# Kernel tuning notes

Measured on AMD Instinct MI355X. Metric: run time of the kernel, lower is better.

Reference implementation:

```python
import jax, jax.numpy as jnp
import numpy as np

CONSTRAINT_WEIGHT = 0.5
FOCAL_GAMMA = 2.0
EPS = 1e-8

B, G, C = 65536, 9, 9
BLK = 3  # int(sqrt(G))


def setup_inputs() -> dict:
    key = jax.random.key(0)
    k1, k2, k3 = jax.random.split(key, 3)
    logits = jax.random.normal(k1, (B, G, G, C), dtype=jnp.float32)
    targets = jax.random.randint(k2, (B, G, G), 0, 10, dtype=jnp.int64)
    puzzles = jax.random.randint(k3, (B, G, G), 0, 10, dtype=jnp.int64)
    return {"logits": logits, "targets": targets, "puzzles": puzzles}


def _sudoku_loss(logits, targets, puzzles):
    b, g, _, c = logits.shape
    mask = (puzzles == 0).astype(logits.dtype)            # [B,G,G]
    tgt = jnp.clip(targets - 1, 0, c - 1)                 # [B,G,G]

    log_probs = jax.nn.log_softmax(logits, axis=-1)       # [B,G,G,C]
    probs = jnp.exp(log_probs)

    # --- focal CE over masked (empty) cells ---
    lp_t = jnp.take_along_axis(log_probs, tgt[..., None], axis=-1)[..., 0]  # [B,G,G]
    pt = jnp.exp(lp_t)
    ce = -lp_t
    focal = (1.0 - pt) ** FOCAL_GAMMA * ce
    msum = mask.sum()
    ce_loss = (focal * mask).sum() / (msum + EPS)

    # --- constraint loss ---
    masked_probs = probs * mask[..., None]                # [B,G,G,C]
    row_sums = masked_probs.sum(axis=2)                   # [B,G,C]
    row_loss = jnp.mean((row_sums - 1.0) ** 2)
    col_sums = masked_probs.sum(axis=1)                   # [B,G,C]
    col_loss = jnp.mean((col_sums - 1.0) ** 2)
    # boxes: [B, br, r, bc, c_in, C] -> sum over the 3x3 cells of each box
    box = masked_probs.reshape(b, BLK, BLK, BLK, BLK, c)
    box_sums = box.transpose(0, 1, 3, 2, 4, 5).reshape(b, BLK * BLK, BLK * BLK, c).sum(axis=2)
    box_loss = jnp.mean((box_sums - 1.0) ** 2)

    entropy = -(probs * log_probs).sum(axis=-1)           # [B,G,G]
    entropy_loss = 0.1 * ((entropy * mask).sum() / (msum + EPS))

    top2, _ = jax.lax.top_k(probs, 2)                     # [B,G,G,2]
    gap = top2[..., 0] - top2[..., 1]
    uniqueness_loss = 0.1 * jnp.mean(jax.nn.relu(1.0 - gap))

    constraint_loss = (row_loss + col_loss + box_loss + entropy_loss + uniqueness_loss) * 0.2
    return ce_loss + CONSTRAINT_WEIGHT * constraint_loss


def reference(logits, targets, puzzles):
    return _sudoku_loss(logits, targets, puzzles)
```

## Files before the change

kernel.cpp:

```cpp
#include <hip/hip_runtime.h>

#define THREADS 256
#define PB 12
#define CELLS_PB (PB * 81)
#define WORKERS 243
#define TOTW (CELLS_PB * 9)

typedef float f4 __attribute__((ext_vector_type(4)));
typedef __fp16 h2 __attribute__((ext_vector_type(2)));
typedef unsigned int u32;
typedef int i4 __attribute__((ext_vector_type(4)));

static __device__ __forceinline__ u32 pkrtz(float a, float b) {
  h2 v = __builtin_amdgcn_cvt_pkrtz(a, b);
  return __builtin_bit_cast(u32, v);
}

__global__ __launch_bounds__(THREADS) void sudoku_main(
    const float* __restrict__ logits,
    const int*   __restrict__ targets,
    const int*   __restrict__ puzzles,
    float* __restrict__ partial,
    int B, int ngrid)
{
  __shared__ float buf[TOTW];
  __shared__ float sred[4][5];

  const int tid = threadIdx.x;
  const int g   = blockIdx.x;
  const long totalCells = (long)B * 81;

  float a_focal=0.f, a_ent=0.f, a_msk=0.f, a_uniq=0.f, a_sq=0.f;

  if (tid < WORKERS) {
    const size_t gbase4 = (size_t)g * (TOTW / 4);
    const size_t lim4   = (size_t)(totalCells * 9 / 4);
    const f4* src = (const f4*)logits;
#pragma unroll
    for (int r = 0; r < 9; ++r) {
      size_t idx = gbase4 + r * WORKERS + tid;
      if (idx < lim4) ((f4*)buf)[r * WORKERS + tid] = src[idx];
    }
  }

  const long cell0 = (long)g * CELLS_PB + 4 * tid;
  const bool vA = (tid < WORKERS) && (cell0 < totalCells);
  i4 tg4{}, pz4{};
  if (vA) {
    tg4 = *(const i4*)(targets + cell0);
    pz4 = *(const i4*)(puzzles + cell0);
  }
  __syncthreads();

  if (vA) {
    f4 s[9];
#pragma unroll
    for (int q = 0; q < 9; ++q) s[q] = ((const f4*)buf)[tid * 9 + q];

#pragma unroll
    for (int k = 0; k < 4; ++k) {
      float l[9];
#pragma unroll
      for (int i = 0; i < 9; ++i) { const int w = 9 * k + i; l[i] = s[w >> 2][w & 3]; }
      int tg = tg4[k] - 1; tg = tg < 0 ? 0 : (tg > 8 ? 8 : tg);

      float t1 = l[0], t2 = -3.0e38f;
#pragma unroll
      for (int i = 1; i < 9; ++i) {
        float hi = fmaxf(t1, l[i]);
        float lo = fminf(t1, l[i]);
        t1 = hi; t2 = fmaxf(t2, lo);
      }
      float e[9], ssum = 0.f, lsum = 0.f, ltg = l[0];
#pragma unroll
      for (int i = 0; i < 9; ++i) {
        float x  = l[i] - t1;
        float ei = __expf(x);
        e[i] = ei; ssum += ei;
        lsum = fmaf(ei, x, lsum);
        if (i > 0) ltg = (tg == i) ? l[i] : ltg;
      }
      float inv_s = __builtin_amdgcn_rcpf(ssum);
      float logs  = __logf(ssum);
      float lpt   = (ltg - t1) - logs;
      float pt    = __expf(lpt);
      float om    = 1.f - pt;
      float focal = om * om * (-lpt);
      float ent   = logs - lsum * inv_s;
      float gap   = (1.f - __expf(t2 - t1)) * inv_s;
      float uq    = fmaxf(0.f, 1.f - gap);
      float mk    = (pz4[k] == 0) ? 1.f : 0.f;
      a_focal += focal * mk;
      a_ent   += ent * mk;
      a_msk   += mk;
      a_uniq  += uq;
      float pm = inv_s * mk;

      u32* pw = (u32*)buf + (size_t)(4 * tid + k) * 9;
      pw[0] = pkrtz(e[0] * pm, e[1] * pm);
      pw[1] = pkrtz(e[2] * pm, e[3] * pm);
      pw[2] = pkrtz(e[4] * pm, e[5] * pm);
      pw[3] = pkrtz(e[6] * pm, e[7] * pm);
      pw[4] = pkrtz(e[8] * pm, 0.f);
    }
  }
  __syncthreads();

  if (tid < PB * 5) {
    const int pz = tid / 5, pr = tid - 5 * pz;
    if ((long)g * PB + pz < B) {
      const u32* cb = (const u32*)buf;
      h2 hz; hz[0] = (__fp16)0.f; hz[1] = (__fp16)0.f;
      h2 rs[9], cs[9], bs[9];
#pragma unroll
      for (int u = 0; u < 9; ++u) { rs[u] = hz; cs[u] = hz; bs[u] = hz; }
      const int base = pz * 729 + pr;
#pragma unroll
      for (int j = 0; j < 81; ++j) {
        h2 v = __builtin_bit_cast(h2, cb[base + 9 * j]);
        rs[j / 9]                    += v;
        cs[j % 9]                    += v;
        bs[(j / 27) * 3 + (j % 9) / 3] += v;
      }
      const float hiw = (pr == 4) ? 0.f : 1.f;
      float sq = 0.f;
#pragma unroll
      for (int u = 0; u < 9; ++u) {
        float x;
        x = (float)rs[u][0] - 1.f; sq = fmaf(x, x, sq);
        x = (float)cs[u][0] - 1.f; sq = fmaf(x, x, sq);
        x = (float)bs[u][0] - 1.f; sq = fmaf(x, x, sq);
        x = (float)rs[u][1] - 1.f; sq = fmaf(hiw * x, x, sq);
        x = (float)cs[u][1] - 1.f; sq = fmaf(hiw * x, x, sq);
        x = (float)bs[u][1] - 1.f; sq = fmaf(hiw * x, x, sq);
      }
      a_sq += sq;
    }
  }

#pragma unroll
  for (int off = 32; off > 0; off >>= 1) {
    a_focal += __shfl_down(a_focal, off);
    a_ent   += __shfl_down(a_ent,   off);
    a_msk   += __shfl_down(a_msk,   off);
    a_uniq  += __shfl_down(a_uniq,  off);
    a_sq    += __shfl_down(a_sq,    off);
  }
  const int wv = tid >> 6, lane = tid & 63;
  if (lane == 0) {
    sred[wv][0] = a_focal; sred[wv][1] = a_ent; sred[wv][2] = a_msk;
    sred[wv][3] = a_uniq;  sred[wv][4] = a_sq;
  }
  __syncthreads();
  if (tid < 5) {
    float v = sred[0][tid] + sred[1][tid] + sred[2][tid] + sred[3][tid];
    partial[(size_t)tid * ngrid + g] = v;
  }
}

__global__ __launch_bounds__(1024) void sudoku_finalize(
    const float* __restrict__ partial, float* __restrict__ out,
    int ngrid, float invBG)
{
  __shared__ float sb[16][5];
  const int tid = threadIdx.x;
  float s[5] = {0.f, 0.f, 0.f, 0.f, 0.f};
  for (int b = tid; b < ngrid; b += 1024) {
#pragma unroll
    for (int u = 0; u < 5; ++u) s[u] += partial[(size_t)u * ngrid + b];
  }
#pragma unroll
  for (int off = 32; off > 0; off >>= 1)
#pragma unroll
    for (int u = 0; u < 5; ++u) s[u] += __shfl_down(s[u], off);
  const int wv = tid >> 6, lane = tid & 63;
  if (lane == 0) {
#pragma unroll
    for (int u = 0; u < 5; ++u) sb[wv][u] = s[u];
  }
  __syncthreads();
  if (tid == 0) {
    float focal = 0.f, ent = 0.f, msum = 0.f, uniq = 0.f, sq = 0.f;
#pragma unroll
    for (int w = 0; w < 16; ++w) {
      focal += sb[w][0]; ent += sb[w][1]; msum += sb[w][2];
      uniq  += sb[w][3]; sq  += sb[w][4];
    }
    float inv_m = 1.f / (msum + 1e-8f);
    float ce    = focal * inv_m;
    float entl  = 0.1f * ent * inv_m;
    float uql   = 0.1f * uniq * invBG;
    float rcb   = sq * invBG;
    float constraint = (rcb + entl + uql) * 0.2f;
    out[0] = ce + 0.5f * constraint;
  }
}

extern "C" void kernel_launch(void* const* d_in, const int* in_sizes, int n_in,
                              void* d_out, int out_size, void* d_ws, size_t ws_size,
                              hipStream_t stream)
{
  (void)n_in; (void)out_size; (void)ws_size;
  const float* logits  = (const float*)d_in[0];
  const int*   targets = (const int*)d_in[1];
  const int*   puzzles = (const int*)d_in[2];
  float* out = (float*)d_out;
  float* partial = (float*)d_ws;

  const int B = in_sizes[0] / 729;
  const long totalCells = (long)B * 81;
  const int ngrid = (int)((totalCells + CELLS_PB - 1) / CELLS_PB);

  sudoku_main<<<ngrid, THREADS, 0, stream>>>(logits, targets, puzzles, partial, B, ngrid);

  const float invBG = 1.f / ((float)B * 81.f);
  sudoku_finalize<<<1, 1024, 0, stream>>>(partial, out, ngrid, invBG);
}
```

Baseline: 57.20 us.

## Replace LDS staging with per-row lane mapping and wavefront shuffle reductions

Each wavefront lane now owns one puzzle row (9 cells) and loads its logits straight from global memory, dropping the shared-memory staging buffer and both block barriers. Row sums are done in registers. Column and box sums use packed-fp16 shuffle-down reductions across lanes. The trade-off is unaligned, strided per-lane loads (each lane reads a 324-byte row segment), which coalesce less well than the old linear f4 copy. It also adds high register pressure (45 packed halves per lane), one idle lane per wave, and many cross-lane shuffles.

```diff
diff --git a/kernel.cpp b/kernel.cpp
--- a/kernel.cpp
+++ b/kernel.cpp
@@ -1,19 +1,28 @@
 #include <hip/hip_runtime.h>
 
 #define THREADS 256
-#define PB 12
-#define CELLS_PB (PB * 81)
-#define WORKERS 243
-#define TOTW (CELLS_PB * 9)
+#define WPP 7
 
 typedef float f4 __attribute__((ext_vector_type(4)));
+typedef f4 f4a4 __attribute__((aligned(4)));
+typedef int i4 __attribute__((ext_vector_type(4)));
+typedef i4 i4a4 __attribute__((aligned(4)));
 typedef __fp16 h2 __attribute__((ext_vector_type(2)));
 typedef unsigned int u32;
-typedef int i4 __attribute__((ext_vector_type(4)));
-
-static __device__ __forceinline__ u32 pkrtz(float a, float b) {
-  h2 v = __builtin_amdgcn_cvt_pkrtz(a, b);
-  return __builtin_bit_cast(u32, v);
+
+static __device__ __forceinline__ h2 shd_h2(h2 v, int d) {
+  u32 x = __builtin_bit_cast(u32, v);
+  x = __shfl_down(x, d);
+  return __builtin_bit_cast(h2, x);
+}
+static __device__ __forceinline__ h2 red9(h2 v) {
+  h2 t = v + shd_h2(v, 1);
+  t = t + shd_h2(t, 2);
+  t = t + shd_h2(t, 4);
+  return t + shd_h2(v, 8);
+}
+static __device__ __forceinline__ h2 red3(h2 v) {
+  return v + shd_h2(v, 1) + shd_h2(v, 2);
 }
 
 __global__ __launch_bounds__(THREADS) void sudoku_main(
@@ -21,48 +30,43 @@
     const int*   __restrict__ targets,
     const int*   __restrict__ puzzles,
     float* __restrict__ partial,
-    int B, int ngrid)
+    int B, int nblk)
 {
-  __shared__ float buf[TOTW];
   __shared__ float sred[4][5];
 
-  const int tid = threadIdx.x;
-  const int g   = blockIdx.x;
-  const long totalCells = (long)B * 81;
+  const int tid  = threadIdx.x;
+  const int wv   = tid >> 6, lane = tid & 63;
+  const long wpass = (long)blockIdx.x * 4 + wv;
+  const int o    = lane % 9;
+  const int pzl  = lane / 9;
+  const long pzG = wpass * WPP + pzl;
+  const bool valid = (lane < 63) && (pzG < (long)B);
 
   float a_focal=0.f, a_ent=0.f, a_msk=0.f, a_uniq=0.f, a_sq=0.f;
 
-  if (tid < WORKERS) {
-    const size_t gbase4 = (size_t)g * (TOTW / 4);
-    const size_t lim4   = (size_t)(totalCells * 9 / 4);
-    const f4* src = (const f4*)logits;
-#pragma unroll
-    for (int r = 0; r < 9; ++r) {
-      size_t idx = gbase4 + r * WORKERS + tid;
-      if (idx < lim4) ((f4*)buf)[r * WORKERS + tid] = src[idx];
-    }
-  }
-
-  const long cell0 = (long)g * CELLS_PB + 4 * tid;
-  const bool vA = (tid < WORKERS) && (cell0 < totalCells);
-  i4 tg4{}, pz4{};
-  if (vA) {
-    tg4 = *(const i4*)(targets + cell0);
-    pz4 = *(const i4*)(puzzles + cell0);
-  }
-  __syncthreads();
-
-  if (vA) {
-    f4 s[9];
-#pragma unroll
-    for (int q = 0; q < 9; ++q) s[q] = ((const f4*)buf)[tid * 9 + q];
-
-#pragma unroll
-    for (int k = 0; k < 4; ++k) {
-      float l[9];
-#pragma unroll
-      for (int i = 0; i < 9; ++i) { const int w = 9 * k + i; l[i] = s[w >> 2][w & 3]; }
-      int tg = tg4[k] - 1; tg = tg < 0 ? 0 : (tg > 8 ? 8 : tg);
+  h2 p45[45];
+  {
+    h2 hz; hz[0] = (__fp16)0.f; hz[1] = (__fp16)0.f;
+#pragma unroll
+    for (int i = 0; i < 45; ++i) p45[i] = hz;
+  }
+
+  if (valid) {
+    const long cellBase = pzG * 81 + (long)o * 9;
+    const float* fb = logits + cellBase * 9;
+    const int*  tb  = targets + cellBase;
+    const int*  pb  = puzzles + cellBase;
+    i4 tg0 = *(const i4a4*)tb, tg1 = *(const i4a4*)(tb + 4);
+    i4 pz0 = *(const i4a4*)pb, pz1 = *(const i4a4*)(pb + 4);
+    const int tgs[9] = {tg0[0],tg0[1],tg0[2],tg0[3],tg1[0],tg1[1],tg1[2],tg1[3],tb[8]};
+    const int pzs[9] = {pz0[0],pz0[1],pz0[2],pz0[3],pz1[0],pz1[1],pz1[2],pz1[3],pb[8]};
+
+#pragma unroll
+    for (int k = 0; k < 9; ++k) {
+      f4 va = *(const f4a4*)(fb + 9 * k);
+      f4 vb = *(const f4a4*)(fb + 9 * k + 4);
+      float l[9] = {va[0],va[1],va[2],va[3],vb[0],vb[1],vb[2],vb[3], fb[9*k+8]};
+      int tg = tgs[k] - 1; tg = tg < 0 ? 0 : (tg > 8 ? 8 : tg);
 
       float t1 = l[0], t2 = -3.0e38f;
 #pragma unroll
@@ -89,52 +93,53 @@
       float ent   = logs - lsum * inv_s;
       float gap   = (1.f - __expf(t2 - t1)) * inv_s;
       float uq    = fmaxf(0.f, 1.f - gap);
-      float mk    = (pz4[k] == 0) ? 1.f : 0.f;
+      float mk    = (pzs[k] == 0) ? 1.f : 0.f;
       a_focal += focal * mk;
       a_ent   += ent * mk;
       a_msk   += mk;
       a_uniq  += uq;
       float pm = inv_s * mk;
-
-      u32* pw = (u32*)buf + (size_t)(4 * tid + k) * 9;
-      pw[0] = pkrtz(e[0] * pm, e[1] * pm);
-      pw[1] = pkrtz(e[2] * pm, e[3] * pm);
-      pw[2] = pkrtz(e[4] * pm, e[5] * pm);
-      pw[3] = pkrtz(e[6] * pm, e[7] * pm);
-      pw[4] = pkrtz(e[8] * pm, 0.f);
-    }
-  }
-  __syncthreads();
-
-  if (tid < PB * 5) {
-    const int pz = tid / 5, pr = tid - 5 * pz;
-    if ((long)g * PB + pz < B) {
-      const u32* cb = (const u32*)buf;
-      h2 hz; hz[0] = (__fp16)0.f; hz[1] = (__fp16)0.f;
-      h2 rs[9], cs[9], bs[9];
-#pragma unroll
-      for (int u = 0; u < 9; ++u) { rs[u] = hz; cs[u] = hz; bs[u] = hz; }
-      const int base = pz * 729 + pr;
-#pragma unroll
-      for (int j = 0; j < 81; ++j) {
-        h2 v = __builtin_bit_cast(h2, cb[base + 9 * j]);
-        rs[j / 9]                    += v;
-        cs[j % 9]                    += v;
-        bs[(j / 27) * 3 + (j % 9) / 3] += v;
-      }
-      const float hiw = (pr == 4) ? 0.f : 1.f;
-      float sq = 0.f;
-#pragma unroll
-      for (int u = 0; u < 9; ++u) {
-        float x;
-        x = (float)rs[u][0] - 1.f; sq = fmaf(x, x, sq);
-        x = (float)cs[u][0] - 1.f; sq = fmaf(x, x, sq);
-        x = (float)bs[u][0] - 1.f; sq = fmaf(x, x, sq);
-        x = (float)rs[u][1] - 1.f; sq = fmaf(hiw * x, x, sq);
-        x = (float)cs[u][1] - 1.f; sq = fmaf(hiw * x, x, sq);
-        x = (float)bs[u][1] - 1.f; sq = fmaf(hiw * x, x, sq);
-      }
-      a_sq += sq;
+      h2 hpm = __builtin_amdgcn_cvt_pkrtz(pm, pm);
+      p45[5*k+0] = __builtin_amdgcn_cvt_pkrtz(e[0], e[1]) * hpm;
+      p45[5*k+1] = __builtin_amdgcn_cvt_pkrtz(e[2], e[3]) * hpm;
+      p45[5*k+2] = __builtin_amdgcn_cvt_pkrtz(e[4], e[5]) * hpm;
+      p45[5*k+3] = __builtin_amdgcn_cvt_pkrtz(e[6], e[7]) * hpm;
+      p45[5*k+4] = __builtin_amdgcn_cvt_pkrtz(e[8], 0.f)  * hpm;
+    }
+
+#pragma unroll
+    for (int j = 0; j < 5; ++j) {
+      h2 s = p45[j];
+#pragma unroll
+      for (int c = 1; c < 9; ++c) s = s + p45[5*c+j];
+      float x = (float)s[0] - 1.f; a_sq = fmaf(x, x, a_sq);
+      if (j < 4) { float y = (float)s[1] - 1.f; a_sq = fmaf(y, y, a_sq); }
+    }
+  }
+
+  h2 bx[15];
+#pragma unroll
+  for (int b = 0; b < 3; ++b)
+#pragma unroll
+    for (int j = 0; j < 5; ++j)
+      bx[b*5+j] = p45[(3*b)*5+j] + p45[(3*b+1)*5+j] + p45[(3*b+2)*5+j];
+#pragma unroll
+  for (int i = 0; i < 15; ++i) bx[i] = red3(bx[i]);
+  if (valid && (o == 0 || o == 3 || o == 6)) {
+#pragma unroll
+    for (int i = 0; i < 15; ++i) {
+      float x = (float)bx[i][0] - 1.f; a_sq = fmaf(x, x, a_sq);
+      if ((i % 5) < 4) { float y = (float)bx[i][1] - 1.f; a_sq = fmaf(y, y, a_sq); }
+    }
+  }
+
+#pragma unroll
+  for (int i = 0; i < 45; ++i) p45[i] = red9(p45[i]);
+  if (valid && o == 0) {
+#pragma unroll
+    for (int i = 0; i < 45; ++i) {
+      float x = (float)p45[i][0] - 1.f; a_sq = fmaf(x, x, a_sq);
+      if ((i % 5) < 4) { float y = (float)p45[i][1] - 1.f; a_sq = fmaf(y, y, a_sq); }
     }
   }
 
@@ -146,7 +151,6 @@
     a_uniq  += __shfl_down(a_uniq,  off);
     a_sq    += __shfl_down(a_sq,    off);
   }
-  const int wv = tid >> 6, lane = tid & 63;
   if (lane == 0) {
     sred[wv][0] = a_focal; sred[wv][1] = a_ent; sred[wv][2] = a_msk;
     sred[wv][3] = a_uniq;  sred[wv][4] = a_sq;
@@ -154,20 +158,20 @@
   __syncthreads();
   if (tid < 5) {
     float v = sred[0][tid] + sred[1][tid] + sred[2][tid] + sred[3][tid];
-    partial[(size_t)tid * ngrid + g] = v;
+    partial[(size_t)tid * nblk + blockIdx.x] = v;
   }
 }
 
 __global__ __launch_bounds__(1024) void sudoku_finalize(
     const float* __restrict__ partial, float* __restrict__ out,
-    int ngrid, float invBG)
+    int nblk, float invBG)
 {
   __shared__ float sb[16][5];
   const int tid = threadIdx.x;
   float s[5] = {0.f, 0.f, 0.f, 0.f, 0.f};
-  for (int b = tid; b < ngrid; b += 1024) {
-#pragma unroll
-    for (int u = 0; u < 5; ++u) s[u] += partial[(size_t)u * ngrid + b];
+  for (int b = tid; b < nblk; b += 1024) {
+#pragma unroll
+    for (int u = 0; u < 5; ++u) s[u] += partial[(size_t)u * nblk + b];
   }
 #pragma unroll
   for (int off = 32; off > 0; off >>= 1)
@@ -208,11 +212,11 @@
   float* partial = (float*)d_ws;
 
   const int B = in_sizes[0] / 729;
-  const long totalCells = (long)B * 81;
-  const int ngrid = (int)((totalCells + CELLS_PB - 1) / CELLS_PB);
-
-  sudoku_main<<<ngrid, THREADS, 0, stream>>>(logits, targets, puzzles, partial, B, ngrid);
+  const long npass = ((long)B + WPP - 1) / WPP;
+  const int  nblk  = (int)((npass + 3) / 4);
+
+  sudoku_main<<<nblk, THREADS, 0, stream>>>(logits, targets, puzzles, partial, B, nblk);
 
   const float invBG = 1.f / ((float)B * 81.f);
-  sudoku_finalize<<<1, 1024, 0, stream>>>(partial, out, ngrid, invBG);
-}
+  sudoku_finalize<<<1, 1024, 0, stream>>>(partial, out, nblk, invBG);
+}
```

After: 69.86 us. +22.1%, slower.

## Convert to persistent grid-stride kernel with double-buffered register-prefetched logits

Applied to the files above, without the earlier changes.

Replaces one-block-per-12-puzzles launch with a persistent grid (capped at 1536 blocks) that loops over 4-puzzle chunks. Logits, targets and puzzles for the next chunk are loaded into registers while the current chunk is computed, then written to the alternate shared buffer. The constraint reduction rotates across waves per iteration. This aims to overlap global memory latency with compute and shrink the shared footprint for higher occupancy, but adds more barriers per unit of work and smaller per-iteration parallelism.

```diff
diff --git a/kernel.cpp b/kernel.cpp
--- a/kernel.cpp
+++ b/kernel.cpp
@@ -1,15 +1,18 @@
 #include <hip/hip_runtime.h>
 
 #define THREADS 256
-#define PB 12
-#define CELLS_PB (PB * 81)
-#define WORKERS 243
-#define TOTW (CELLS_PB * 9)
+#define CPZ 4
+#define CC (CPZ * 81)
+#define CW (CC * 9)
+#define CF4 (CW / 4)
+#define MAXG 1536
 
 typedef float f4 __attribute__((ext_vector_type(4)));
+typedef float f2 __attribute__((ext_vector_type(2)));
+typedef int   i2 __attribute__((ext_vector_type(2)));
 typedef __fp16 h2 __attribute__((ext_vector_type(2)));
 typedef unsigned int u32;
-typedef int i4 __attribute__((ext_vector_type(4)));
+typedef u32 u2 __attribute__((ext_vector_type(2)));
 
 static __device__ __forceinline__ u32 pkrtz(float a, float b) {
   h2 v = __builtin_amdgcn_cvt_pkrtz(a, b);
@@ -21,121 +24,160 @@
     const int*   __restrict__ targets,
     const int*   __restrict__ puzzles,
     float* __restrict__ partial,
-    int B, int ngrid)
+    int B, long nchunk, int grid)
 {
-  __shared__ float buf[TOTW];
+  __shared__ float buf[2][CW];
   __shared__ float sred[4][5];
 
-  const int tid = threadIdx.x;
-  const int g   = blockIdx.x;
+  const int tid  = threadIdx.x;
+  const int wv   = tid >> 6, lane = tid & 63;
   const long totalCells = (long)B * 81;
+  const long totF4      = totalCells * 9 / 4;
+  const bool stager  = tid < 243;
 
   float a_focal=0.f, a_ent=0.f, a_msk=0.f, a_uniq=0.f, a_sq=0.f;
 
-  if (tid < WORKERS) {
-    const size_t gbase4 = (size_t)g * (TOTW / 4);
-    const size_t lim4   = (size_t)(totalCells * 9 / 4);
+  const long c0 = blockIdx.x;
+  if (stager) {
     const f4* src = (const f4*)logits;
-#pragma unroll
-    for (int r = 0; r < 9; ++r) {
-      size_t idx = gbase4 + r * WORKERS + tid;
-      if (idx < lim4) ((f4*)buf)[r * WORKERS + tid] = src[idx];
-    }
-  }
-
-  const long cell0 = (long)g * CELLS_PB + 4 * tid;
-  const bool vA = (tid < WORKERS) && (cell0 < totalCells);
-  i4 tg4{}, pz4{};
-  if (vA) {
-    tg4 = *(const i4*)(targets + cell0);
-    pz4 = *(const i4*)(puzzles + cell0);
-  }
-  __syncthreads();
-
-  if (vA) {
-    f4 s[9];
-#pragma unroll
-    for (int q = 0; q < 9; ++q) s[q] = ((const f4*)buf)[tid * 9 + q];
-
-#pragma unroll
-    for (int k = 0; k < 4; ++k) {
-      float l[9];
-#pragma unroll
-      for (int i = 0; i < 9; ++i) { const int w = 9 * k + i; l[i] = s[w >> 2][w & 3]; }
-      int tg = tg4[k] - 1; tg = tg < 0 ? 0 : (tg > 8 ? 8 : tg);
-
-      float t1 = l[0], t2 = -3.0e38f;
-#pragma unroll
-      for (int i = 1; i < 9; ++i) {
-        float hi = fmaxf(t1, l[i]);
-        float lo = fminf(t1, l[i]);
-        t1 = hi; t2 = fmaxf(t2, lo);
+    const long b4 = c0 * CF4;
+#pragma unroll
+    for (int r = 0; r < 3; ++r) {
+      long idx = b4 + r * 243 + tid;
+      if (idx < totF4) ((f4*)buf[0])[r * 243 + tid] = src[idx];
+    }
+  }
+  bool vA = false; i2 tgc{}, pzc{};
+  {
+    const long cell0 = c0 * CC + 2 * tid;
+    vA = (tid < 162) && (cell0 + 1 < totalCells);
+    if (vA) { tgc = *(const i2*)(targets + cell0); pzc = *(const i2*)(puzzles + cell0); }
+  }
+
+  int it = 0;
+  for (long c = c0; c < nchunk; c += grid, ++it) {
+    float* X = buf[it & 1];
+    float* Y = buf[(it & 1) ^ 1];
+    __syncthreads();
+
+    const long cn = c + grid;
+    f4 r0{}, r1{}, r2{};
+    const bool vS = stager && (cn < nchunk);
+    if (vS) {
+      const f4* src = (const f4*)logits;
+      const long b4 = cn * CF4;
+      long i0 = b4 + tid, i1 = b4 + 243 + tid, ii2 = b4 + 486 + tid;
+      if (i0  < totF4) r0 = src[i0];
+      if (i1  < totF4) r1 = src[i1];
+      if (ii2 < totF4) r2 = src[ii2];
+    }
+    bool vAn = false; i2 tgn{}, pzn{};
+    if (cn < nchunk) {
+      const long cell0n = cn * CC + 2 * tid;
+      vAn = (tid < 162) && (cell0n + 1 < totalCells);
+      if (vAn) { tgn = *(const i2*)(targets + cell0n); pzn = *(const i2*)(puzzles + cell0n); }
+    }
+
+    if (vA) {
+      f2 v[9];
+      const f2* xp = (const f2*)(X + 18 * tid);
+#pragma unroll
+      for (int q = 0; q < 9; ++q) v[q] = xp[q];
+
+      u32 q5[2][5];
+#pragma unroll
+      for (int k = 0; k < 2; ++k) {
+        float l[9];
+#pragma unroll
+        for (int i = 0; i < 9; ++i) { const int w = 9 * k + i; l[i] = v[w >> 1][w & 1]; }
+        int tg = ((k == 0) ? tgc[0] : tgc[1]) - 1; tg = tg < 0 ? 0 : (tg > 8 ? 8 : tg);
+        const int pz = (k == 0) ? pzc[0] : pzc[1];
+
+        float t1 = l[0], t2 = -3.0e38f;
+#pragma unroll
+        for (int i = 1; i < 9; ++i) {
+          float hi = fmaxf(t1, l[i]);
+          float lo = fminf(t1, l[i]);
+          t1 = hi; t2 = fmaxf(t2, lo);
+        }
+        float e[9], ssum = 0.f, lsum = 0.f, ltg = l[0];
+#pragma unroll
+        for (int i = 0; i < 9; ++i) {
+          float x  = l[i] - t1;
+          float ei = __expf(x);
+          e[i] = ei; ssum += ei;
+          lsum = fmaf(ei, x, lsum);
+          if (i > 0) ltg = (tg == i) ? l[i] : ltg;
+        }
+        float inv_s = __builtin_amdgcn_rcpf(ssum);
+        float logs  = __logf(ssum);
+        float lpt   = (ltg - t1) - logs;
+        float pt    = __expf(lpt);
+        float om    = 1.f - pt;
+        float focal = om * om * (-lpt);
+        float ent   = logs - lsum * inv_s;
+        float gap   = (1.f - __expf(t2 - t1)) * inv_s;
+        float uq    = fmaxf(0.f, 1.f - gap);
+        float mk    = (pz == 0) ? 1.f : 0.f;
+        a_focal += focal * mk;
+        a_ent   += ent * mk;
+        a_msk   += mk;
+        a_uniq  += uq;
+        float pm = inv_s * mk;
+        q5[k][0] = pkrtz(e[0]*pm, e[1]*pm);
+        q5[k][1] = pkrtz(e[2]*pm, e[3]*pm);
+        q5[k][2] = pkrtz(e[4]*pm, e[5]*pm);
+        q5[k][3] = pkrtz(e[6]*pm, e[7]*pm);
+        q5[k][4] = pkrtz(e[8]*pm, 0.f);
       }
-      float e[9], ssum = 0.f, lsum = 0.f, ltg = l[0];
-#pragma unroll
-      for (int i = 0; i < 9; ++i) {
-        float x  = l[i] - t1;
-        float ei = __expf(x);
-        e[i] = ei; ssum += ei;
-        lsum = fmaf(ei, x, lsum);
-        if (i > 0) ltg = (tg == i) ? l[i] : ltg;
+      u32* wp = (u32*)(X + 18 * tid);
+      { u2 a; a[0]=q5[0][0]; a[1]=q5[0][1]; *(u2*)(wp + 0) = a; }
+      { u2 a; a[0]=q5[0][2]; a[1]=q5[0][3]; *(u2*)(wp + 2) = a; }
+      wp[4] = q5[0][4];
+      wp[9] = q5[1][0];
+      { u2 a; a[0]=q5[1][1]; a[1]=q5[1][2]; *(u2*)(wp + 10) = a; }
+      { u2 a; a[0]=q5[1][3]; a[1]=q5[1][4]; *(u2*)(wp + 12) = a; }
+    }
+
+    if (vS) {
+      f4* yp = (f4*)Y;
+      yp[tid] = r0; yp[243 + tid] = r1; yp[486 + tid] = r2;
+    }
+    __syncthreads();
+
+    if (wv == (it & 3) && lane < CPZ * 5) {
+      const int pzl = lane / 5, pr = lane % 5;
+      if (c * CPZ + pzl < (long)B) {
+        const u32* cb = (const u32*)X;
+        h2 hz; hz[0] = (__fp16)0.f; hz[1] = (__fp16)0.f;
+        h2 rs[9], cs[9], bs[9];
+#pragma unroll
+        for (int u = 0; u < 9; ++u) { rs[u] = hz; cs[u] = hz; bs[u] = hz; }
+        const int base = pzl * 729 + pr;
+#pragma unroll
+        for (int j = 0; j < 81; ++j) {
+          h2 pv = __builtin_bit_cast(h2, cb[base + 9 * j]);
+          rs[j / 9]                      += pv;
+          cs[j % 9]                      += pv;
+          bs[(j / 27) * 3 + (j % 9) / 3] += pv;
+        }
+        const float hiw = (pr == 4) ? 0.f : 1.f;
+        float sq = 0.f;
+#pragma unroll
+        for (int u = 0; u < 9; ++u) {
+          float x;
+          x = (float)rs[u][0] - 1.f; sq = fmaf(x, x, sq);
+          x = (float)cs[u][0] - 1.f; sq = fmaf(x, x, sq);
+          x = (float)bs[u][0] - 1.f; sq = fmaf(x, x, sq);
+          x = (float)rs[u][1] - 1.f; sq = fmaf(hiw * x, x, sq);
+          x = (float)cs[u][1] - 1.f; sq = fmaf(hiw * x, x, sq);
+          x = (float)bs[u][1] - 1.f; sq = fmaf(hiw * x, x, sq);
+        }
+        a_sq += sq;
       }
-      float inv_s = __builtin_amdgcn_rcpf(ssum);
-      float logs  = __logf(ssum);
-      float lpt   = (ltg - t1) - logs;
-      float pt    = __expf(lpt);
-      float om    = 1.f - pt;
-      float focal = om * om * (-lpt);
-      float ent   = logs - lsum * inv_s;
-      float gap   = (1.f - __expf(t2 - t1)) * inv_s;
-      float uq    = fmaxf(0.f, 1.f - gap);
-      float mk    = (pz4[k] == 0) ? 1.f : 0.f;
-      a_focal += focal * mk;
-      a_ent   += ent * mk;
-      a_msk   += mk;
-      a_uniq  += uq;
-      float pm = inv_s * mk;
-
-      u32* pw = (u32*)buf + (size_t)(4 * tid + k) * 9;
-      pw[0] = pkrtz(e[0] * pm, e[1] * pm);
-      pw[1] = pkrtz(e[2] * pm, e[3] * pm);
-      pw[2] = pkrtz(e[4] * pm, e[5] * pm);
-      pw[3] = pkrtz(e[6] * pm, e[7] * pm);
-      pw[4] = pkrtz(e[8] * pm, 0.f);
-    }
-  }
-  __syncthreads();
-
-  if (tid < PB * 5) {
-    const int pz = tid / 5, pr = tid - 5 * pz;
-    if ((long)g * PB + pz < B) {
-      const u32* cb = (const u32*)buf;
-      h2 hz; hz[0] = (__fp16)0.f; hz[1] = (__fp16)0.f;
-      h2 rs[9], cs[9], bs[9];
-#pragma unroll
-      for (int u = 0; u < 9; ++u) { rs[u] = hz; cs[u] = hz; bs[u] = hz; }
-      const int base = pz * 729 + pr;
-#pragma unroll
-      for (int j = 0; j < 81; ++j) {
-        h2 v = __builtin_bit_cast(h2, cb[base + 9 * j]);
-        rs[j / 9]                    += v;
-        cs[j % 9]                    += v;
-        bs[(j / 27) * 3 + (j % 9) / 3] += v;
-      }
-      const float hiw = (pr == 4) ? 0.f : 1.f;
-      float sq = 0.f;
-#pragma unroll
-      for (int u = 0; u < 9; ++u) {
-        float x;
-        x = (float)rs[u][0] - 1.f; sq = fmaf(x, x, sq);
-        x = (float)cs[u][0] - 1.f; sq = fmaf(x, x, sq);
-        x = (float)bs[u][0] - 1.f; sq = fmaf(x, x, sq);
-        x = (float)rs[u][1] - 1.f; sq = fmaf(hiw * x, x, sq);
-        x = (float)cs[u][1] - 1.f; sq = fmaf(hiw * x, x, sq);
-        x = (float)bs[u][1] - 1.f; sq = fmaf(hiw * x, x, sq);
-      }
-      a_sq += sq;
-    }
+    }
+
+    vA = vAn; tgc = tgn; pzc = pzn;
   }
 
 #pragma unroll
@@ -146,7 +188,6 @@
     a_uniq  += __shfl_down(a_uniq,  off);
     a_sq    += __shfl_down(a_sq,    off);
   }
-  const int wv = tid >> 6, lane = tid & 63;
   if (lane == 0) {
     sred[wv][0] = a_focal; sred[wv][1] = a_ent; sred[wv][2] = a_msk;
     sred[wv][3] = a_uniq;  sred[wv][4] = a_sq;
@@ -154,20 +195,20 @@
   __syncthreads();
   if (tid < 5) {
     float v = sred[0][tid] + sred[1][tid] + sred[2][tid] + sred[3][tid];
-    partial[(size_t)tid * ngrid + g] = v;
+    partial[(size_t)tid * grid + blockIdx.x] = v;
   }
 }
 
 __global__ __launch_bounds__(1024) void sudoku_finalize(
     const float* __restrict__ partial, float* __restrict__ out,
-    int ngrid, float invBG)
+    int nblk, float invBG)
 {
   __shared__ float sb[16][5];
   const int tid = threadIdx.x;
   float s[5] = {0.f, 0.f, 0.f, 0.f, 0.f};
-  for (int b = tid; b < ngrid; b += 1024) {
-#pragma unroll
-    for (int u = 0; u < 5; ++u) s[u] += partial[(size_t)u * ngrid + b];
+  for (int b = tid; b < nblk; b += 1024) {
+#pragma unroll
+    for (int u = 0; u < 5; ++u) s[u] += partial[(size_t)u * nblk + b];
   }
 #pragma unroll
   for (int off = 32; off > 0; off >>= 1)
@@ -208,11 +249,12 @@
   float* partial = (float*)d_ws;
 
   const int B = in_sizes[0] / 729;
-  const long totalCells = (long)B * 81;
-  const int ngrid = (int)((totalCells + CELLS_PB - 1) / CELLS_PB);
-
-  sudoku_main<<<ngrid, THREADS, 0, stream>>>(logits, targets, puzzles, partial, B, ngrid);
+  const long nchunk = ((long)B + CPZ - 1) / CPZ;
+  const int grid = (int)(nchunk < MAXG ? nchunk : MAXG);
+
+  sudoku_main<<<grid, THREADS, 0, stream>>>(logits, targets, puzzles, partial,
+                                            B, nchunk, grid);
 
   const float invBG = 1.f / ((float)B * 81.f);
-  sudoku_finalize<<<1, 1024, 0, stream>>>(partial, out, ngrid, invBG);
-}
+  sudoku_finalize<<<1, 1024, 0, stream>>>(partial, out, grid, invBG);
+}
```

New measurement: 73.03 us. 1.28x slower.

## Use persistent blocks with double-buffered async global-to-LDS loads

Applied to the files above, without the earlier changes.

Replaces the one-block-per-chunk launch with a persistent grid capped at 512 blocks. Each block loops over chunks and double-buffers LDS, issuing global_load_lds for the next chunk while computing the current one, with manual vmcnt waits. The goal is to overlap memory traffic with compute and to cut the block count and the partials the finalize kernel reads. The cost is more LDS per block (two padded buffers), which lowers occupancy, plus fragile hand-written waitcnt counting.

```diff
diff --git a/kernel.cpp b/kernel.cpp
--- a/kernel.cpp
+++ b/kernel.cpp
@@ -3,8 +3,10 @@
 #define THREADS 256
 #define PB 12
 #define CELLS_PB (PB * 81)
-#define WORKERS 243
-#define TOTW (CELLS_PB * 9)
+#define CHW (CELLS_PB * 9)
+#define CHF4 (CHW / 4)
+#define PADF4 2304
+#define MAXG 512
 
 typedef float f4 __attribute__((ext_vector_type(4)));
 typedef __fp16 h2 __attribute__((ext_vector_type(2)));
@@ -15,48 +17,55 @@
   h2 v = __builtin_amdgcn_cvt_pkrtz(a, b);
   return __builtin_bit_cast(u32, v);
 }
-
-__global__ __launch_bounds__(THREADS) void sudoku_main(
-    const float* __restrict__ logits,
-    const int*   __restrict__ targets,
-    const int*   __restrict__ puzzles,
-    float* __restrict__ partial,
-    int B, int ngrid)
-{
-  __shared__ float buf[TOTW];
-  __shared__ float sred[4][5];
-
-  const int tid = threadIdx.x;
-  const int g   = blockIdx.x;
-  const long totalCells = (long)B * 81;
-
-  float a_focal=0.f, a_ent=0.f, a_msk=0.f, a_uniq=0.f, a_sq=0.f;
-
-  if (tid < WORKERS) {
-    const size_t gbase4 = (size_t)g * (TOTW / 4);
-    const size_t lim4   = (size_t)(totalCells * 9 / 4);
-    const f4* src = (const f4*)logits;
+static __device__ __forceinline__ void gload_lds16(const f4* g, f4* l) {
+  __builtin_amdgcn_global_load_lds(
+      (const __attribute__((address_space(1))) void*)g,
+      (__attribute__((address_space(3))) void*)l, 16, 0, 0);
+}
+#define WAITV11() do { asm volatile("s_waitcnt vmcnt(11)" ::: "memory"); \
+                       __builtin_amdgcn_sched_barrier(0); } while (0)
+#define WAITV0()  do { asm volatile("s_waitcnt vmcnt(0)"  ::: "memory"); \
+                       __builtin_amdgcn_sched_barrier(0); } while (0)
+#define WAITL0()  do { asm volatile("s_waitcnt lgkmcnt(0)" ::: "memory"); \
+                       __builtin_amdgcn_sched_barrier(0); } while (0)
+#define BAR()     do { asm volatile("" ::: "memory"); __builtin_amdgcn_s_barrier(); \
+                       asm volatile("" ::: "memory"); \
+                       __builtin_amdgcn_sched_barrier(0); } while (0)
+
+static __device__ __forceinline__ void issue_chunk(
+    const f4* __restrict__ src, const int* __restrict__ targets,
+    const int* __restrict__ puzzles, f4* lbuf, long c, long totF4,
+    long maxCell0, int tid, i4& tg4, i4& pz4)
+{
+  const long b4 = c * CHF4;
+  if (b4 + PADF4 <= totF4) {
+#pragma unroll
+    for (int r = 0; r < 9; ++r)
+      gload_lds16(src + b4 + r * 256 + tid, lbuf + r * 256 + tid);
+  } else {
+    const long lim = totF4 - 1;
 #pragma unroll
     for (int r = 0; r < 9; ++r) {
-      size_t idx = gbase4 + r * WORKERS + tid;
-      if (idx < lim4) ((f4*)buf)[r * WORKERS + tid] = src[idx];
-    }
-  }
-
-  const long cell0 = (long)g * CELLS_PB + 4 * tid;
-  const bool vA = (tid < WORKERS) && (cell0 < totalCells);
-  i4 tg4{}, pz4{};
-  if (vA) {
-    tg4 = *(const i4*)(targets + cell0);
-    pz4 = *(const i4*)(puzzles + cell0);
-  }
-  __syncthreads();
-
-  if (vA) {
+      long idx = b4 + r * 256 + tid;
+      idx = idx < lim ? idx : lim;
+      gload_lds16(src + idx, lbuf + r * 256 + tid);
+    }
+  }
+  long cell0 = c * CELLS_PB + 4 * tid;
+  cell0 = cell0 < maxCell0 ? cell0 : maxCell0;
+  tg4 = *(const i4*)(targets + cell0);
+  pz4 = *(const i4*)(puzzles + cell0);
+}
+
+static __device__ __forceinline__ void phaseA(
+    f4* lbuf, const i4& tg4, const i4& pz4, long c, long totalCells, int tid,
+    float& a_focal, float& a_ent, float& a_msk, float& a_uniq)
+{
+  const long rem = totalCells - c * CELLS_PB;
+  if (tid < 243 && (long)(4 * tid) < rem) {
     f4 s[9];
 #pragma unroll
-    for (int q = 0; q < 9; ++q) s[q] = ((const f4*)buf)[tid * 9 + q];
-
+    for (int q = 0; q < 9; ++q) s[q] = lbuf[tid * 9 + q];
 #pragma unroll
     for (int k = 0; k < 4; ++k) {
       float l[9];
@@ -96,7 +105,7 @@
       a_uniq  += uq;
       float pm = inv_s * mk;
 
-      u32* pw = (u32*)buf + (size_t)(4 * tid + k) * 9;
+      u32* pw = (u32*)lbuf + (size_t)(4 * tid + k) * 9;
       pw[0] = pkrtz(e[0] * pm, e[1] * pm);
       pw[1] = pkrtz(e[2] * pm, e[3] * pm);
       pw[2] = pkrtz(e[4] * pm, e[5] * pm);
@@ -104,12 +113,15 @@
       pw[4] = pkrtz(e[8] * pm, 0.f);
     }
   }
-  __syncthreads();
-
+}
+
+static __device__ __forceinline__ void phaseC(
+    const f4* lbuf, long c, int B, int tid, float& a_sq)
+{
   if (tid < PB * 5) {
     const int pz = tid / 5, pr = tid - 5 * pz;
-    if ((long)g * PB + pz < B) {
-      const u32* cb = (const u32*)buf;
+    if (c * PB + pz < (long)B) {
+      const u32* cb = (const u32*)lbuf;
       h2 hz; hz[0] = (__fp16)0.f; hz[1] = (__fp16)0.f;
       h2 rs[9], cs[9], bs[9];
 #pragma unroll
@@ -118,8 +130,8 @@
 #pragma unroll
       for (int j = 0; j < 81; ++j) {
         h2 v = __builtin_bit_cast(h2, cb[base + 9 * j]);
-        rs[j / 9]                    += v;
-        cs[j % 9]                    += v;
+        rs[j / 9]                      += v;
+        cs[j % 9]                      += v;
         bs[(j / 27) * 3 + (j % 9) / 3] += v;
       }
       const float hiw = (pr == 4) ? 0.f : 1.f;
@@ -137,7 +149,59 @@
       a_sq += sq;
     }
   }
-
+}
+
+__global__ __launch_bounds__(THREADS) void sudoku_main(
+    const float* __restrict__ logits,
+    const int*   __restrict__ targets,
+    const int*   __restrict__ puzzles,
+    float* __restrict__ partial,
+    int B, long nchunk, int grid)
+{
+  __shared__ f4 bufA[PADF4];
+  __shared__ f4 bufB[PADF4];
+  __shared__ float sred[4][5];
+
+  const int tid = threadIdx.x;
+  const long totalCells = (long)B * 81;
+  const long totF4 = totalCells * 9 / 4;
+  const long maxCell0 = totalCells - 4;
+  const long c0 = blockIdx.x;
+  const long G = grid;
+
+  float a_focal=0.f, a_ent=0.f, a_msk=0.f, a_uniq=0.f, a_sq=0.f;
+  i4 tgA{}, pzA{}, tgB{}, pzB{};
+
+  issue_chunk((const f4*)logits, targets, puzzles, bufA, c0, totF4, maxCell0, tid, tgA, pzA);
+  if (c0 + G < nchunk)
+    issue_chunk((const f4*)logits, targets, puzzles, bufB, c0 + G, totF4, maxCell0, tid, tgB, pzB);
+
+  for (long c = c0; c < nchunk; c += 2 * G) {
+    if (c + G < nchunk) WAITV11(); else WAITV0();
+    BAR();
+    phaseA(bufA, tgA, pzA, c, totalCells, tid, a_focal, a_ent, a_msk, a_uniq);
+    WAITL0(); BAR();
+    phaseC(bufA, c, B, tid, a_sq);
+    WAITL0(); BAR();
+    if (c + 2 * G < nchunk)
+      issue_chunk((const f4*)logits, targets, puzzles, bufA, c + 2 * G,
+                  totF4, maxCell0, tid, tgA, pzA);
+
+    const long cb = c + G;
+    if (cb < nchunk) {
+      if (cb + G < nchunk) WAITV11(); else WAITV0();
+      BAR();
+      phaseA(bufB, tgB, pzB, cb, totalCells, tid, a_focal, a_ent, a_msk, a_uniq);
+      WAITL0(); BAR();
+      phaseC(bufB, cb, B, tid, a_sq);
+      WAITL0(); BAR();
+      if (cb + 2 * G < nchunk)
+        issue_chunk((const f4*)logits, targets, puzzles, bufB, cb + 2 * G,
+                    totF4, maxCell0, tid, tgB, pzB);
+    }
+  }
+
+  const int wv = tid >> 6, lane = tid & 63;
 #pragma unroll
   for (int off = 32; off > 0; off >>= 1) {
     a_focal += __shfl_down(a_focal, off);
@@ -146,7 +210,6 @@
     a_uniq  += __shfl_down(a_uniq,  off);
     a_sq    += __shfl_down(a_sq,    off);
   }
-  const int wv = tid >> 6, lane = tid & 63;
   if (lane == 0) {
     sred[wv][0] = a_focal; sred[wv][1] = a_ent; sred[wv][2] = a_msk;
     sred[wv][3] = a_uniq;  sred[wv][4] = a_sq;
@@ -154,7 +217,7 @@
   __syncthreads();
   if (tid < 5) {
     float v = sred[0][tid] + sred[1][tid] + sred[2][tid] + sred[3][tid];
-    partial[(size_t)tid * ngrid + g] = v;
+    partial[(size_t)tid * grid + blockIdx.x] = v;
   }
 }
 
@@ -209,10 +272,12 @@
 
   const int B = in_sizes[0] / 729;
   const long totalCells = (long)B * 81;
-  const int ngrid = (int)((totalCells + CELLS_PB - 1) / CELLS_PB);
-
-  sudoku_main<<<ngrid, THREADS, 0, stream>>>(logits, targets, puzzles, partial, B, ngrid);
+  const long nchunk = (totalCells + CELLS_PB - 1) / CELLS_PB;
+  const int grid = (int)(nchunk < MAXG ? nchunk : MAXG);
+
+  sudoku_main<<<grid, THREADS, 0, stream>>>(logits, targets, puzzles, partial,
+                                            B, nchunk, grid);
 
   const float invBG = 1.f / ((float)B * 81.f);
-  sudoku_finalize<<<1, 1024, 0, stream>>>(partial, out, ngrid, invBG);
-}
+  sudoku_finalize<<<1, 1024, 0, stream>>>(partial, out, grid, invBG);
+}
```

New measurement: 68.45 us. 19.7% more time.
